# Performance work log

Measured on AMD Instinct MI355X. Metric: run time of the kernel, lower is better.

The kernel has to match this reference:

```python
import jax, jax.numpy as jnp
import numpy as np

N = 4194304  # number of 3D points (surfels)
H, W = 1024, 1280


def setup_inputs() -> dict:
    key = jax.random.key(0)
    k1, k2, k3 = jax.random.split(key, 3)
    # camera-frame points: x,y in [-0.5, 0.5], z (depth) in [0.5, 2.5]
    xy = jax.random.uniform(k1, (N, 2), dtype=jnp.float32, minval=-0.5, maxval=0.5)
    z = jax.random.uniform(k2, (N, 1), dtype=jnp.float32, minval=0.5, maxval=2.5)
    points = jnp.concatenate([xy, z], axis=-1)
    colors = jax.random.uniform(k3, (N, 3), dtype=jnp.float32)
    fx = fy = 1000.0
    K = jnp.array([[fx, 0.0, W / 2.0], [0.0, fy, H / 2.0], [0.0, 0.0, 1.0]],
                  dtype=jnp.float32)
    return {"points": points, "colors": colors, "K": K, "height": H, "width": W}


def reference(points, colors, K, height, width):
    # pcd2depth: pinhole projection with rounding
    fx, fy, cx, cy = K[0, 0], K[1, 1], K[0, 2], K[1, 2]
    z = points[:, 2]
    u = jnp.round(fx * points[:, 0] / z + cx).astype(jnp.int32)
    v = jnp.round(fy * points[:, 1] / z + cy).astype(jnp.int32)
    valid = (z > 0) & (u >= 0) & (u < width) & (v >= 0) & (v < height)
    n = points.shape[0]
    npix = height * width
    # sentinel pixel npix for invalid points
    flat = jnp.where(valid, v * width + u, npix)
    # far-to-near overwrite after depth_sort=True)
    order = jnp.argsort(jnp.where(valid, z, jnp.inf))  # ascending depth
    flat_sorted = flat[order]
    ranks = jnp.arange(n, dtype=jnp.int32)
    # per-pixel min rank (rank = position in depth-ascending order)
    win = jnp.full(npix + 1, n, dtype=jnp.int32).at[flat_sorted].min(ranks)
    win = win[:npix]
    has_point = win < n
    winner = order[jnp.minimum(win, n - 1)]  # point index per pixel
    img = jnp.where(has_point[:, None], colors[winner].astype(jnp.float32), 0.0)
    return img.reshape(height, width, 3)
```

## Files before the change

kernel.cpp:

```cpp
#include <hip/hip_runtime.h>
#include <stdint.h>

#define NPTS    4194304
#define IMG_H   1024
#define IMG_W   1280
#define NPIX    (IMG_H * IMG_W)

#define TW      40
#define TH      32
#define TILES_X (IMG_W / TW)
#define TILES_Y (IMG_H / TH)
#define NBINS   (TILES_X * TILES_Y)
#define TPIX    (TW * TH)

#define NBLK    1280
#define TPB     256
#define TPB_R   256
#define SEGS_PER_T (NBLK / TPB_R)
#if (NBLK % TPB_R) != 0
#error "NBLK must be a multiple of TPB_R"
#endif

#define CHUNK_Q ((NPTS / 4 + NBLK - 1) / NBLK)
#define CHUNK_P (CHUNK_Q * 4)
#define SSTRIDE CHUNK_P
#define QPT     ((CHUNK_Q + TPB - 1) / TPB)
#define BPT     (NBINS / TPB)

static const unsigned long long KEY_SENTINEL = ~0ULL;
#define KEY47_MASK ((1ULL << 47) - 1)


struct Perm { unsigned short p[NBINS]; };
constexpr Perm make_perm() {
    unsigned short rank[NBINS] = {};
    float score[NBINS] = {};
    for (int i = 0; i < NBINS; ++i) {
        int tx = i % TILES_X, ty = i / TILES_X;
        float du = ((float)tx + 0.5f) * (float)TW - 640.0f;
        float dv = ((float)ty + 0.5f) * (float)TH - 512.0f;
        du /= 640.0f; dv /= 512.0f;
        score[i] = du * du + dv * dv;
        rank[i] = (unsigned short)i;
    }
    for (int i = 1; i < NBINS; ++i) {
        unsigned short key = rank[i];
        float ks = score[key];
        int j = i - 1;
        while (j >= 0 && score[rank[j]] > ks) { rank[j + 1] = rank[j]; --j; }
        rank[j + 1] = key;
    }
    Perm P{};
    for (int i = 0; i < NBINS; ++i) {
        int r = i / 256, k = i % 256;
        int src = (r & 1) ? (r * 256 + (255 - k)) : (r * 256 + k);
        P.p[i] = rank[src];
    }
    return P;
}
__device__ __constant__ Perm c_perm = make_perm();

__device__ __forceinline__ bool project(float x, float y, float z,
                                        float fx, float fy, float cx, float cy,
                                        int& u, int& v) {
    float uf = rintf(fx * x / z + cx);
    float vf = rintf(fy * y / z + cy);
    bool valid = (z > 0.0f) &&
                 (uf >= 0.0f) && (uf < (float)IMG_W) &&
                 (vf >= 0.0f) && (vf < (float)IMG_H);
    u = (int)uf;
    v = (int)vf;
    return valid;
}

__device__ __forceinline__ unsigned int zc_of(float z) {
    unsigned int zb = __float_as_uint(z);
    unsigned int zc = zb - 0x3F000000u;
    if ((int)zc < 0) zc = 0;
    if (zc > 0x1FFFFFFu) zc = 0x1FFFFFFu;
    return zc;
}

__global__ __launch_bounds__(TPB, 4) void pass_bin(
        const float4* __restrict__ pts4, const float* __restrict__ Kmat,
        unsigned int* __restrict__ cnt_off ,
        unsigned long long* __restrict__ grec ,
        int n_quads, int qchunk) {
    __shared__ unsigned long long srec[CHUNK_P];
    __shared__ unsigned int hist[NBINS];
    __shared__ unsigned int cur[NBINS];
    __shared__ unsigned int tsum[TPB];

    int t   = threadIdx.x;
    int blk = blockIdx.x;
#pragma unroll
    for (int i = t; i < NBINS; i += TPB) hist[i] = 0;
    __syncthreads();

    float fx = Kmat[0], cx = Kmat[2];
    float fy = Kmat[4], cy = Kmat[5];

    int q0 = blk * qchunk;
    int q1 = min(n_quads, q0 + qchunk);

    unsigned long long keep[QPT * 4];

#pragma unroll
    for (int qi = 0; qi < QPT; ++qi) {
        int q = q0 + t + qi * TPB;
        bool inb = (q < q1);
        float4 a = {}, b = {}, c = {};
        if (inb) {
            a = pts4[3 * q + 0];
            b = pts4[3 * q + 1];
            c = pts4[3 * q + 2];
        }
        float px[4] = {a.x, a.w, b.z, c.y};
        float py[4] = {a.y, b.x, b.w, c.z};
        float pz[4] = {a.z, b.y, c.x, c.w};
#pragma unroll
        for (int k = 0; k < 4; ++k) {
            unsigned long long kv = ~0ULL;
            int u, v;
            if (inb && project(px[k], py[k], pz[k], fx, fy, cx, cy, u, v)) {
                int tx  = u / TW;
                int bin = (v >> 5) * TILES_X + tx;
                unsigned int pos = (unsigned int)((v & 31) * TW + (u - tx * TW));
                atomicAdd(&hist[bin], 1u);
                kv = ((unsigned long long)bin << 36) |
                     ((unsigned long long)pos << 25) |
                     (unsigned long long)zc_of(pz[k]);
            }
            keep[qi * 4 + k] = kv;
        }
    }
    __syncthreads();

    unsigned int hv[BPT];
    {
        unsigned int s = 0;
#pragma unroll
        for (int j = 0; j < BPT; ++j) { hv[j] = hist[BPT * t + j]; s += hv[j]; }
        tsum[t] = s;
    }
    __syncthreads();
    for (int off = 1; off < TPB; off <<= 1) {
        unsigned int x = (t >= off) ? tsum[t - off] : 0u;
        __syncthreads();
        tsum[t] += x;
        __syncthreads();
    }
    {
        unsigned int run = (t > 0) ? tsum[t - 1] : 0u;
#pragma unroll
        for (int j = 0; j < BPT; ++j) {
            cur[BPT * t + j] = run;
            run += hv[j];
        }
    }
    __syncthreads();

#pragma unroll
    for (int i = t; i < NBINS; i += TPB)
        cnt_off[(size_t)blk * NBINS + i] = (hist[i] << 16) | cur[i];
    __syncthreads();

#pragma unroll
    for (int qi = 0; qi < QPT; ++qi) {
        int q = q0 + t + qi * TPB;
        unsigned int i0 = 4u * (unsigned int)q;
#pragma unroll
        for (int k = 0; k < 4; ++k) {
            unsigned long long kv = keep[qi * 4 + k];
            if (kv != ~0ULL) {
                int bin          = (int)(kv >> 36);
                unsigned int pos = (unsigned int)((kv >> 25) & 0x7FFu);
                unsigned int zc  = (unsigned int)(kv & 0x1FFFFFFu);
                unsigned int slot = atomicAdd(&cur[bin], 1u);
                srec[slot] = ((unsigned long long)pos << 47) |
                             ((unsigned long long)zc << 22) |
                             (unsigned long long)(i0 + (unsigned int)k);
            }
        }
    }
    __syncthreads();

    unsigned int nrec = cur[NBINS - 1];
    unsigned long long* my = grec + (size_t)blk * SSTRIDE;
    for (unsigned int i = t; i < nrec; i += TPB) my[i] = srec[i];
}

__global__ __launch_bounds__(256) void transpose_table(
        const unsigned int* __restrict__ in ,
        unsigned int* __restrict__ outT     ) {
    __shared__ unsigned int tile[32][33];
    int t  = threadIdx.x;
    int tx = t & 31, ty = t >> 5;
    int bx = blockIdx.x % (NBINS / 32);
    int by = blockIdx.x / (NBINS / 32);
#pragma unroll
    for (int i = 0; i < 4; ++i) {
        int r = by * 32 + ty + i * 8;
        tile[ty + i * 8][tx] = in[(size_t)r * NBINS + (bx * 32 + tx)];
    }
    __syncthreads();
#pragma unroll
    for (int i = 0; i < 4; ++i) {
        int r = bx * 32 + ty + i * 8;
        outT[(size_t)r * NBLK + (by * 32 + tx)] = tile[tx][ty + i * 8];
    }
}

__global__ __launch_bounds__(TPB_R) void pass_render(
        const unsigned long long* __restrict__ grec,
        const unsigned int* __restrict__ cnt_offT ,
        const float* __restrict__ colors,
        float* __restrict__ out, int npts) {
    __shared__ unsigned long long key[TPIX];

    int t = threadIdx.x;
    int b = c_perm.p[blockIdx.x];

#pragma unroll
    for (int i = t; i < TPIX; i += TPB_R) key[i] = KEY_SENTINEL;

    unsigned int w[SEGS_PER_T];
#pragma unroll
    for (int s = 0; s < SEGS_PER_T; ++s)
        w[s] = cnt_offT[(size_t)b * NBLK + (t + s * TPB_R)];
    __syncthreads();

#pragma unroll
    for (int s = 0; s < SEGS_PER_T; ++s) {
        unsigned int cnt = w[s] >> 16;
        unsigned int off = w[s] & 0xFFFFu;
        const unsigned long long* seg =
            grec + (size_t)(t + s * TPB_R) * SSTRIDE + off;
        if ((off & 1u) && cnt) {
            unsigned long long rec = seg[0];
            atomicMin(&key[(unsigned int)(rec >> 47)], rec & KEY47_MASK);
            ++seg; --cnt;
        }
        const ulonglong2* seg2 = (const ulonglong2*)seg;
        unsigned int np = cnt >> 1;
        unsigned int p = 0;
        for (; p + 2 <= np; p += 2) {
            ulonglong2 a  = seg2[p];
            ulonglong2 b2 = seg2[p + 1];
            atomicMin(&key[(unsigned int)(a.x  >> 47)], a.x  & KEY47_MASK);
            atomicMin(&key[(unsigned int)(a.y  >> 47)], a.y  & KEY47_MASK);
            atomicMin(&key[(unsigned int)(b2.x >> 47)], b2.x & KEY47_MASK);
            atomicMin(&key[(unsigned int)(b2.y >> 47)], b2.y & KEY47_MASK);
        }
        if (p < np) {
            ulonglong2 a = seg2[p];
            atomicMin(&key[(unsigned int)(a.x >> 47)], a.x & KEY47_MASK);
            atomicMin(&key[(unsigned int)(a.y >> 47)], a.y & KEY47_MASK);
        }
        if (cnt & 1u) {
            unsigned long long rec = seg[cnt - 1];
            atomicMin(&key[(unsigned int)(rec >> 47)], rec & KEY47_MASK);
        }
    }
    __syncthreads();

    int tx = b % TILES_X, ty = b / TILES_X;
#pragma unroll
    for (int i = t; i < TPIX; i += TPB_R) {
        int row = i / TW, col = i - row * TW;
        unsigned long long kk = key[i];
        float r = 0.0f, g = 0.0f, bl = 0.0f;
        if (kk != KEY_SENTINEL) {
            unsigned int idx = (unsigned int)(kk & 0x3FFFFFu);
            if (idx + 1u < (unsigned int)npts) {
                float4 c4 = *(const float4*)(colors + 3u * idx);
                r = c4.x; g = c4.y; bl = c4.z;
            } else {
                r  = colors[3u * idx + 0];
                g  = colors[3u * idx + 1];
                bl = colors[3u * idx + 2];
            }
        }
        size_t gp = (size_t)(ty * TH + row) * IMG_W + (size_t)(tx * TW + col);
        out[3 * gp + 0] = r;
        out[3 * gp + 1] = g;
        out[3 * gp + 2] = bl;
    }
}

__global__ void init_keys_vec(ulonglong2* __restrict__ keys, int n_vec2) {
    int i = blockIdx.x * blockDim.x + threadIdx.x;
    if (i < n_vec2) keys[i] = ulonglong2{~0ULL, ~0ULL};
}

__global__ void scatter_points_pretest(const float4* __restrict__ pts4,
                                       const float* __restrict__ Kmat,
                                       unsigned long long* __restrict__ keys,
                                       int n_quads) {
    int t = blockIdx.x * blockDim.x + threadIdx.x;
    if (t >= n_quads) return;
    float fx = Kmat[0], cx = Kmat[2];
    float fy = Kmat[4], cy = Kmat[5];
    float4 a = pts4[3 * t + 0];
    float4 b = pts4[3 * t + 1];
    float4 c = pts4[3 * t + 2];
    float px[4] = {a.x, a.w, b.z, c.y};
    float py[4] = {a.y, b.x, b.w, c.z};
    float pz[4] = {a.z, b.y, c.x, c.w};
    unsigned int i0 = 4u * (unsigned int)t;
#pragma unroll
    for (int k = 0; k < 4; ++k) {
        int u, v;
        if (!project(px[k], py[k], pz[k], fx, fy, cx, cy, u, v)) continue;
        int pix = v * IMG_W + u;
        unsigned long long key =
            ((unsigned long long)__float_as_uint(pz[k]) << 32) | (i0 + k);
        if (key < keys[pix]) atomicMin(&keys[pix], key);
    }
}

__global__ void resolve_pixels4(const unsigned long long* __restrict__ keys,
                                const float* __restrict__ colors,
                                float* __restrict__ out, int n_quads) {
    int t = blockIdx.x * blockDim.x + threadIdx.x;
    if (t >= n_quads) return;
    int base = 4 * t;
    ulonglong2 k01 = *(const ulonglong2*)(keys + base);
    ulonglong2 k23 = *(const ulonglong2*)(keys + base + 2);
    unsigned long long kk[4] = {k01.x, k01.y, k23.x, k23.y};
    float c[12];
#pragma unroll
    for (int j = 0; j < 4; ++j) {
        float r = 0.0f, g = 0.0f, b = 0.0f;
        if (kk[j] != KEY_SENTINEL) {
            unsigned int idx = (unsigned int)(kk[j] & 0xFFFFFFFFu);
            r = colors[3 * idx + 0];
            g = colors[3 * idx + 1];
            b = colors[3 * idx + 2];
        }
        c[3 * j + 0] = r; c[3 * j + 1] = g; c[3 * j + 2] = b;
    }
    float4* o = (float4*)(out + 3 * (size_t)base);
    o[0] = float4{c[0], c[1], c[2],  c[3]};
    o[1] = float4{c[4], c[5], c[6],  c[7]};
    o[2] = float4{c[8], c[9], c[10], c[11]};
}

extern "C" void kernel_launch(void* const* d_in, const int* in_sizes, int n_in,
                              void* d_out, int out_size, void* d_ws, size_t ws_size,
                              hipStream_t stream) {
    const float4* pts4  = (const float4*)d_in[0];
    const float* colors = (const float*)d_in[1];
    const float* Kmat   = (const float*)d_in[2];
    float* out = (float*)d_out;

    int n       = in_sizes[0] / 3;
    int n_quads = n / 4;
    int qchunk  = (n_quads + NBLK - 1) / NBLK;

    char* ws = (char*)d_ws;
    size_t off = 0;
    auto alloc = [&](size_t bytes) {
        char* p = ws + off;
        off += (bytes + 63) & ~(size_t)63;
        return p;
    };
    unsigned int*       cnt_off  = (unsigned int*)alloc((size_t)NBLK * NBINS * 4);
    unsigned int*       cnt_offT = (unsigned int*)alloc((size_t)NBLK * NBINS * 4);
    unsigned long long* grec =
        (unsigned long long*)alloc((size_t)NBLK * SSTRIDE * 8);

    if (qchunk <= CHUNK_Q && ws_size >= off) {
        pass_bin<<<NBLK, TPB, 0, stream>>>(pts4, Kmat, cnt_off, grec,
                                           n_quads, qchunk);
        transpose_table<<<(NBINS / 32) * (NBLK / 32), 256, 0, stream>>>(
            cnt_off, cnt_offT);
        pass_render<<<NBINS, TPB_R, 0, stream>>>(grec, cnt_offT, colors, out, n);
    } else {
        unsigned long long* keys = (unsigned long long*)d_ws;
        const int B = 256;
        int n_vec2 = NPIX / 2;
        init_keys_vec<<<(n_vec2 + B - 1) / B, B, 0, stream>>>(
            (ulonglong2*)keys, n_vec2);
        scatter_points_pretest<<<(n_quads + B - 1) / B, B, 0, stream>>>(
            pts4, Kmat, keys, n_quads);
        int npix_quads = NPIX / 4;
        resolve_pixels4<<<(npix_quads + B - 1) / B, B, 0, stream>>>(
            keys, colors, out, npix_quads);
    }
}
```

Measured before the change: 169.1 us.

## Split 64-bit depth-index atomicMin into two 32-bit passes and shrink binning grid

The render pass replaces the single 64-bit shared-memory atomicMin on a packed depth|index key with two 32-bit passes. The first finds the minimum depth code per pixel, and the second re-reads the segment records and atomically takes the minimum index only among records matching that depth. This avoids 64-bit LDS atomics but reads the binned records from global memory twice. Separately, the binning block count drops from 1280 to 768, with launch bounds lowered to 3 waves per SIMD, which means larger per-block chunks and more shared memory per block.

Result: slower. 184.7 us (+9.3%).

```diff
diff --git a/kernel.cpp b/kernel.cpp
--- a/kernel.cpp
+++ b/kernel.cpp
@@ -13,7 +13,7 @@
 #define NBINS   (TILES_X * TILES_Y)
 #define TPIX    (TW * TH)
 
-#define NBLK    1280
+#define NBLK    768
 #define TPB     256
 #define TPB_R   256
 #define SEGS_PER_T (NBLK / TPB_R)
@@ -81,7 +81,7 @@
     return zc;
 }
 
-__global__ __launch_bounds__(TPB, 4) void pass_bin(
+__global__ __launch_bounds__(TPB, 3) void pass_bin(
         const float4* __restrict__ pts4, const float* __restrict__ Kmat,
         unsigned int* __restrict__ cnt_off ,
         unsigned long long* __restrict__ grec ,
@@ -216,13 +216,14 @@
         const unsigned int* __restrict__ cnt_offT ,
         const float* __restrict__ colors,
         float* __restrict__ out, int npts) {
-    __shared__ unsigned long long key[TPIX];
+    __shared__ unsigned int zmin32[TPIX];
+    __shared__ unsigned int imin32[TPIX];
 
     int t = threadIdx.x;
     int b = c_perm.p[blockIdx.x];
 
 #pragma unroll
-    for (int i = t; i < TPIX; i += TPB_R) key[i] = KEY_SENTINEL;
+    for (int i = t; i < TPIX; i += TPB_R) { zmin32[i] = ~0u; imin32[i] = ~0u; }
 
     unsigned int w[SEGS_PER_T];
 #pragma unroll
@@ -238,7 +239,8 @@
             grec + (size_t)(t + s * TPB_R) * SSTRIDE + off;
         if ((off & 1u) && cnt) {
             unsigned long long rec = seg[0];
-            atomicMin(&key[(unsigned int)(rec >> 47)], rec & KEY47_MASK);
+            atomicMin(&zmin32[(unsigned int)(rec >> 47)],
+                      (unsigned int)(rec >> 22) & 0x1FFFFFFu);
             ++seg; --cnt;
         }
         const ulonglong2* seg2 = (const ulonglong2*)seg;
@@ -247,19 +249,54 @@
         for (; p + 2 <= np; p += 2) {
             ulonglong2 a  = seg2[p];
             ulonglong2 b2 = seg2[p + 1];
-            atomicMin(&key[(unsigned int)(a.x  >> 47)], a.x  & KEY47_MASK);
-            atomicMin(&key[(unsigned int)(a.y  >> 47)], a.y  & KEY47_MASK);
-            atomicMin(&key[(unsigned int)(b2.x >> 47)], b2.x & KEY47_MASK);
-            atomicMin(&key[(unsigned int)(b2.y >> 47)], b2.y & KEY47_MASK);
+            atomicMin(&zmin32[(unsigned int)(a.x  >> 47)], (unsigned int)(a.x  >> 22) & 0x1FFFFFFu);
+            atomicMin(&zmin32[(unsigned int)(a.y  >> 47)], (unsigned int)(a.y  >> 22) & 0x1FFFFFFu);
+            atomicMin(&zmin32[(unsigned int)(b2.x >> 47)], (unsigned int)(b2.x >> 22) & 0x1FFFFFFu);
+            atomicMin(&zmin32[(unsigned int)(b2.y >> 47)], (unsigned int)(b2.y >> 22) & 0x1FFFFFFu);
         }
         if (p < np) {
             ulonglong2 a = seg2[p];
-            atomicMin(&key[(unsigned int)(a.x >> 47)], a.x & KEY47_MASK);
-            atomicMin(&key[(unsigned int)(a.y >> 47)], a.y & KEY47_MASK);
+            atomicMin(&zmin32[(unsigned int)(a.x >> 47)], (unsigned int)(a.x >> 22) & 0x1FFFFFFu);
+            atomicMin(&zmin32[(unsigned int)(a.y >> 47)], (unsigned int)(a.y >> 22) & 0x1FFFFFFu);
         }
         if (cnt & 1u) {
             unsigned long long rec = seg[cnt - 1];
-            atomicMin(&key[(unsigned int)(rec >> 47)], rec & KEY47_MASK);
+            atomicMin(&zmin32[(unsigned int)(rec >> 47)],
+                      (unsigned int)(rec >> 22) & 0x1FFFFFFu);
+        }
+    }
+    __syncthreads();
+
+#pragma unroll
+    for (int s = 0; s < SEGS_PER_T; ++s) {
+        unsigned int cnt = w[s] >> 16;
+        unsigned int off = w[s] & 0xFFFFu;
+        const unsigned long long* seg =
+            grec + (size_t)(t + s * TPB_R) * SSTRIDE + off;
+        if ((off & 1u) && cnt) {
+            unsigned long long rec = seg[0];
+            unsigned int pos = (unsigned int)(rec >> 47);
+            if (((unsigned int)(rec >> 22) & 0x1FFFFFFu) == zmin32[pos])
+                atomicMin(&imin32[pos], (unsigned int)rec & 0x3FFFFFu);
+            ++seg; --cnt;
+        }
+        const ulonglong2* seg2 = (const ulonglong2*)seg;
+        unsigned int np = cnt >> 1;
+        unsigned int p = 0;
+        for (; p < np; ++p) {
+            ulonglong2 a = seg2[p];
+            unsigned int posx = (unsigned int)(a.x >> 47);
+            unsigned int posy = (unsigned int)(a.y >> 47);
+            if (((unsigned int)(a.x >> 22) & 0x1FFFFFFu) == zmin32[posx])
+                atomicMin(&imin32[posx], (unsigned int)a.x & 0x3FFFFFu);
+            if (((unsigned int)(a.y >> 22) & 0x1FFFFFFu) == zmin32[posy])
+                atomicMin(&imin32[posy], (unsigned int)a.y & 0x3FFFFFu);
+        }
+        if (cnt & 1u) {
+            unsigned long long rec = seg[cnt - 1];
+            unsigned int pos = (unsigned int)(rec >> 47);
+            if (((unsigned int)(rec >> 22) & 0x1FFFFFFu) == zmin32[pos])
+                atomicMin(&imin32[pos], (unsigned int)rec & 0x3FFFFFu);
         }
     }
     __syncthreads();
@@ -268,10 +305,9 @@
 #pragma unroll
     for (int i = t; i < TPIX; i += TPB_R) {
         int row = i / TW, col = i - row * TW;
-        unsigned long long kk = key[i];
         float r = 0.0f, g = 0.0f, bl = 0.0f;
-        if (kk != KEY_SENTINEL) {
-            unsigned int idx = (unsigned int)(kk & 0x3FFFFFu);
+        if (zmin32[i] != ~0u) {
+            unsigned int idx = imin32[i] & 0x3FFFFFu;
             if (idx + 1u < (unsigned int)npts) {
                 float4 c4 = *(const float4*)(colors + 3u * idx);
                 r = c4.x; g = c4.y; bl = c4.z;
```
